# Optimization experiments

Measured on AMD Instinct MI355X. Metric: run time of the kernel, lower is better.

The kernel has to match this reference:

```python
import jax, jax.numpy as jnp
import numpy as np

# Model config (matches init_kwargs)
DIM = 2048
INTER = 1408          # moe_inter_dim
E = 16                # n_routed_experts
TOPK = 4              # n_activated_experts
G = 4                 # n_expert_groups
TOPK_G = 2            # n_limited_groups
N_SHARED = 2
SHARED_INTER = N_SHARED * INTER  # 2816
ROUTE_SCALE = 1.0


def setup_inputs() -> dict:
    key = jax.random.key(0)
    ks = jax.random.split(key, 8)
    s = 0.02
    x = jax.random.normal(ks[0], (1, 2048, DIM), dtype=jnp.float32)
    Wg = jax.random.normal(ks[1], (E, DIM), dtype=jnp.float32) * s      # gate weight
    W1 = jax.random.normal(ks[2], (E, INTER, DIM), dtype=jnp.float32) * s  # expert gate proj
    W3 = jax.random.normal(ks[3], (E, INTER, DIM), dtype=jnp.float32) * s  # expert up proj
    W2 = jax.random.normal(ks[4], (E, DIM, INTER), dtype=jnp.float32) * s  # expert down proj
    Ws1 = jax.random.normal(ks[5], (SHARED_INTER, DIM), dtype=jnp.float32) * s
    Ws3 = jax.random.normal(ks[6], (SHARED_INTER, DIM), dtype=jnp.float32) * s
    Ws2 = jax.random.normal(ks[7], (DIM, SHARED_INTER), dtype=jnp.float32) * s
    return {"x": x, "Wg": Wg, "W1": W1, "W3": W3, "W2": W2,
            "Ws1": Ws1, "Ws3": Ws3, "Ws2": Ws2}


def _moe_forward(x, Wg, W1, W3, W2, Ws1, Ws3, Ws2):
    B, S, D = x.shape
    xt = x.reshape(-1, D)              # [T, D]
    T = xt.shape[0]

    # ---- Gate: group-limited top-k routing (bias is None since dim != 7168) ----
    scores = jax.nn.softmax(xt @ Wg.T, axis=-1)          # [T, E]
    sg = scores.reshape(T, G, E // G)                    # [T, G, E/G]
    group_scores = sg.max(axis=-1)                       # amax per group
    gidx = jax.lax.top_k(group_scores, TOPK_G)[1]        # [T, TOPK_G]
    gmask = jax.nn.one_hot(gidx, G, dtype=jnp.float32).sum(axis=1) > 0  # [T, G] kept groups
    masked = jnp.where(gmask[:, :, None], sg, -jnp.inf).reshape(T, E)
    topi = jax.lax.top_k(masked, TOPK)[1]                # [T, TOPK] expert indices
    weights = jnp.take_along_axis(scores, topi, axis=1) * ROUTE_SCALE  # original_scores gather

    # ---- Routed experts: dense per-expert SwiGLU FFN, zero-weight combine ----
    # combine[t, e] = sum over k of weights[t, k] * (topi[t, k] == e)
    combine = jnp.zeros((T, E), xt.dtype).at[jnp.arange(T)[:, None], topi].add(weights)
    h = jax.nn.silu(jnp.einsum('td,eid->eti', xt, W1)) * jnp.einsum('td,eid->eti', xt, W3)
    expert_out = jnp.einsum('eti,edi->etd', h, W2)       # [E, T, D]
    y = jnp.einsum('etd,te->td', expert_out, combine)    # [T, D]

    # ---- Shared expert (applied to all tokens) ----
    z = (jax.nn.silu(xt @ Ws1.T) * (xt @ Ws3.T)) @ Ws2.T

    return (y + z).reshape(B, S, D)


def reference(x, Wg, W1, W3, W2, Ws1, Ws3, Ws2):
    return _moe_forward(x, Wg, W1, W3, W2, Ws1, Ws3, Ws2)
```

## Files before the change

### kernel.cpp

```cpp
#include <hip/hip_runtime.h>
#include <stdint.h>

#define D_MODEL  2048
#define N_INTER  1408
#define SH_INTER 2816
#define T_TOK    2048
#define NSLOT    (T_TOK * 4)
#define MIB(x)   ((size_t)(x) << 20)

typedef __attribute__((ext_vector_type(8))) short bf16x8;
typedef __attribute__((ext_vector_type(4))) float f32x4;

__device__ __forceinline__ unsigned short f2bf(float f){
  unsigned int b = __builtin_bit_cast(unsigned int, f);
  b = (b + 0x7FFFu + ((b >> 16) & 1u)) >> 16;
  return (unsigned short)b;
}
__device__ __forceinline__ float bf2f(unsigned short h){
  unsigned int b = ((unsigned int)h) << 16;
  return __builtin_bit_cast(float, b);
}

#define GLOAD16(gp, lp) __builtin_amdgcn_global_load_lds( \
    (const __attribute__((address_space(1))) unsigned int*)(gp), \
    (__attribute__((address_space(3))) unsigned int*)(lp), 16, 0, 0)

__device__ __forceinline__ void cvt_tail(const float* __restrict__ src,
                                         unsigned short* __restrict__ dst,
                                         int n4, int cb, int nblk, int tid){
  const float4* s = (const float4*)src;
  ushort4* d = (ushort4*)dst;
  const int stride = nblk * 256;
  for (int i = cb * 256 + tid; i < n4; i += stride){
    const float4 v = s[i];
    ushort4 u; u.x = f2bf(v.x); u.y = f2bf(v.y); u.z = f2bf(v.z); u.w = f2bf(v.w);
    d[i] = u;
  }
}

__global__ void cvt4_kernel(const float* __restrict__ x,  const float* __restrict__ Ws1,
                            const float* __restrict__ Ws3, const float* __restrict__ Ws2,
                            unsigned short* __restrict__ xbf, unsigned short* __restrict__ S1,
                            unsigned short* __restrict__ S3,  unsigned short* __restrict__ S2){
  const int N0 = T_TOK * D_MODEL / 4;
  const int NW = SH_INTER * D_MODEL / 4;
  const int total = N0 + 3 * NW;
  const int stride = gridDim.x * blockDim.x;
  for (int i = blockIdx.x * blockDim.x + threadIdx.x; i < total; i += stride){
    const float4* s; ushort4* d; int j;
    if (i < N0)            { s = (const float4*)x;   d = (ushort4*)xbf; j = i; }
    else if (i < N0 + NW)  { s = (const float4*)Ws1; d = (ushort4*)S1;  j = i - N0; }
    else if (i < N0 + 2*NW){ s = (const float4*)Ws3; d = (ushort4*)S3;  j = i - N0 - NW; }
    else                   { s = (const float4*)Ws2; d = (ushort4*)S2;  j = i - N0 - 2*NW; }
    const float4 v = s[j];
    ushort4 u; u.x = f2bf(v.x); u.y = f2bf(v.y); u.z = f2bf(v.z); u.w = f2bf(v.w);
    d[j] = u;
  }
}

__global__ void gate_kernel(const float* __restrict__ x, const float* __restrict__ Wg,
                            int* __restrict__ cnt, int* __restrict__ list,
                            float* __restrict__ wslot){
  const int t = blockIdx.x;
  const int l = threadIdx.x;
  const int e = l & 15, q = l >> 4;
  const float* xr = x + (size_t)t * D_MODEL + q * 512;
  const float* wr = Wg + (size_t)e * D_MODEL + q * 512;
  float p = 0.f;
  #pragma unroll 4
  for (int i = 0; i < 512; i += 4){
    float4 xv = *(const float4*)(xr + i);
    float4 wv = *(const float4*)(wr + i);
    p += xv.x*wv.x + xv.y*wv.y + xv.z*wv.z + xv.w*wv.w;
  }
  p += __shfl_xor(p, 16);
  p += __shfl_xor(p, 32);
  float mx = p;
  for (int d = 1; d < 16; d <<= 1) mx = fmaxf(mx, __shfl_xor(mx, d));
  float ex = __expf(p - mx);
  float sum = ex;
  for (int d = 1; d < 16; d <<= 1) sum += __shfl_xor(sum, d);
  const float sc = ex / sum;
  float gm = fmaxf(sc, __shfl_xor(sc, 1));
  gm = fmaxf(gm, __shfl_xor(gm, 2));
  const float g0 = __shfl(gm, 0), g1 = __shfl(gm, 4),
              g2 = __shfl(gm, 8), g3 = __shfl(gm, 12);
  const int grp = e >> 2;
  const float gs[4] = {g0, g1, g2, g3};
  int grank = 0;
  #pragma unroll
  for (int j = 0; j < 4; ++j)
    if (gs[j] > gm || (gs[j] == gm && j < grp)) grank++;
  const float msc = (grank < 2) ? sc : -INFINITY;
  int erank = 0;
  #pragma unroll
  for (int j = 0; j < 16; ++j){
    const float oj = __shfl(msc, j);
    if (oj > msc || (oj == msc && j < e)) erank++;
  }
  if (q == 0 && erank < 4 && msc > -INFINITY){
    const int pos = atomicAdd(&cnt[e], 1);
    const int slot = (t << 2) | erank;
    list[e * T_TOK + pos] = slot;
    wslot[slot] = sc;
  }
}

template<int MODE>
__global__ __launch_bounds__(256, 3)
void gemm6_kernel(const unsigned short* __restrict__ A,
                  const unsigned short* __restrict__ B,
                  void* __restrict__ OutP,
                  const int* __restrict__ list,
                  const int* __restrict__ cnt,
                  int N, int K, int Astride, int MT, int NT,
                  const float* __restrict__ cvtSrc,
                  unsigned short* __restrict__ cvtDst,
                  int cvtN4, int gemmN)
{
  constexpr bool GATHER = (MODE >= 2);
  __shared__ unsigned short As[3 * 128 * 32];
  __shared__ unsigned short Bs[3 * 128 * 32];

  const int tid = threadIdx.x;
  const int bid = blockIdx.x;
  if (bid >= gemmN){
    cvt_tail(cvtSrc, cvtDst, cvtN4, bid - gemmN, gridDim.x - gemmN, tid);
    return;
  }

  const int per = gemmN >> 3;
  const int gsw = (bid & 7) * per + (bid >> 3);
  const int mt   = gsw % MT;
  const int rest = gsw / MT;
  const int nt = GATHER ? (rest % NT) : rest;
  const int e  = GATHER ? (rest / NT) : 0;

  const int cntE = GATHER ? cnt[e] : (MT * 128);
  if (mt * 128 >= cntE) return;

  const int wid = tid >> 6, lane = tid & 63;

  const int rt0 = 32 * wid + (lane >> 2), rt1 = rt0 + 16;
  const int sxA = ((lane & 3) ^ ((lane >> 3) & 3)) << 3;

  int ar0, ar1;
  if constexpr (GATHER){
    const int lim = cntE - 1;
    int p0 = mt * 128 + rt0; p0 = p0 < lim ? p0 : lim;
    int p1 = mt * 128 + rt1; p1 = p1 < lim ? p1 : lim;
    const int e0 = list[e * T_TOK + p0], e1 = list[e * T_TOK + p1];
    ar0 = (MODE == 2) ? (e0 >> 2) : e0;
    ar1 = (MODE == 2) ? (e1 >> 2) : e1;
  } else { ar0 = mt * 128 + rt0; ar1 = mt * 128 + rt1; }

  const unsigned short* pa0 = A + (size_t)ar0 * Astride + sxA;
  const unsigned short* pa1 = A + (size_t)ar1 * Astride + sxA;
  const unsigned short* pb0 = B + (GATHER ? (size_t)e * N * K : 0)
                            + (size_t)(nt * 128 + rt0) * K + sxA;
  const unsigned short* pb1 = pb0 + (size_t)16 * K;

  const int aW0 = (32 * wid) * 32, aW1 = aW0 + 16 * 32;
  const int bufStride = 128 * 32;

  const int wr = wid >> 1, wc = wid & 1, lr = lane & 15, lq = lane >> 4;
  const int fx = ((lq ^ ((lr >> 1) & 3)) << 3);
  int aoff[4], boff[4];
  #pragma unroll
  for (int m = 0; m < 4; ++m) aoff[m] = (wr * 64 + m * 16 + lr) * 32 + fx;
  #pragma unroll
  for (int n = 0; n < 4; ++n) boff[n] = (wc * 64 + n * 16 + lr) * 32 + fx;

  f32x4 acc[4][4];
  const f32x4 zero = {0.f, 0.f, 0.f, 0.f};
  #pragma unroll
  for (int m = 0; m < 4; ++m)
    #pragma unroll
    for (int n = 0; n < 4; ++n) acc[m][n] = zero;

  const int KT = K >> 5;
  #pragma unroll
  for (int t = 0; t < 3; ++t){
    GLOAD16(pa0, As + t * bufStride + aW0);
    GLOAD16(pa1, As + t * bufStride + aW1);
    GLOAD16(pb0, Bs + t * bufStride + aW0);
    GLOAD16(pb1, Bs + t * bufStride + aW1);
    pa0 += 32; pa1 += 32; pb0 += 32; pb1 += 32;
  }
  int c = 0;

  for (int kt = 0; kt < KT; ++kt){
    if (kt < KT - 2)       asm volatile("s_waitcnt vmcnt(8)" ::: "memory");
    else if (kt == KT - 2) asm volatile("s_waitcnt vmcnt(4)" ::: "memory");
    else                   asm volatile("s_waitcnt vmcnt(0)" ::: "memory");
    __builtin_amdgcn_s_barrier();

    const unsigned short* aC = As + c * bufStride;
    const unsigned short* bC = Bs + c * bufStride;
    bf16x8 af[4], bf[4];
    #pragma unroll
    for (int m = 0; m < 4; ++m) af[m] = *(const bf16x8*)(aC + aoff[m]);
    #pragma unroll
    for (int n = 0; n < 4; ++n) bf[n] = *(const bf16x8*)(bC + boff[n]);

    asm volatile("s_waitcnt lgkmcnt(0)" ::: "memory");
    __builtin_amdgcn_sched_barrier(0);
    __builtin_amdgcn_s_barrier();

    if (kt + 3 < KT){
      GLOAD16(pa0, As + c * bufStride + aW0);
      GLOAD16(pa1, As + c * bufStride + aW1);
      GLOAD16(pb0, Bs + c * bufStride + aW0);
      GLOAD16(pb1, Bs + c * bufStride + aW1);
      pa0 += 32; pa1 += 32; pb0 += 32; pb1 += 32;
    }

    #pragma unroll
    for (int n = 0; n < 4; ++n)
      #pragma unroll
      for (int m = 0; m < 4; ++m)
        acc[m][n] = __builtin_amdgcn_mfma_f32_16x16x32_bf16(af[m], bf[n], acc[m][n], 0, 0, 0);

    c = (c == 2) ? 0 : c + 1;
  }

  const int colBase = nt * 128 + wc * 64;
  #pragma unroll
  for (int m = 0; m < 4; ++m){
    #pragma unroll
    for (int r = 0; r < 4; ++r){
      const int grow = mt * 128 + wr * 64 + m * 16 + lq * 4 + r;
      if constexpr (MODE == 1){
        float* op = (float*)OutP + (size_t)grow * N + colBase;
        #pragma unroll
        for (int n = 0; n < 4; ++n) op[n * 16 + lr] = acc[m][n][r];
      } else if constexpr (MODE == 0){
        unsigned short* op = (unsigned short*)OutP + (size_t)grow * N + colBase;
        #pragma unroll
        for (int n = 0; n < 4; ++n) op[n * 16 + lr] = f2bf(acc[m][n][r]);
      } else {
        if (grow >= cntE) continue;
        const int orow = list[e * T_TOK + grow];
        unsigned short* op = (unsigned short*)OutP + (size_t)orow * N + colBase;
        #pragma unroll
        for (int n = 0; n < 4; ++n) op[n * 16 + lr] = f2bf(acc[m][n][r]);
      }
    }
  }
}

__global__ void swiglu_ip_kernel(unsigned short* __restrict__ GU, int n8, int NI8){
  const int stride = gridDim.x * blockDim.x;
  bf16x8* p = (bf16x8*)GU;
  for (int i = blockIdx.x * blockDim.x + threadIdx.x; i < n8; i += stride){
    const int r = i / NI8, ccol = i - r * NI8;
    const size_t gi = (size_t)r * 2 * NI8 + ccol;
    const bf16x8 g = p[gi];
    const bf16x8 u = p[gi + NI8];
    bf16x8 h;
    #pragma unroll
    for (int j = 0; j < 8; ++j){
      const float gv = bf2f((unsigned short)g[j]);
      const float uv = bf2f((unsigned short)u[j]);
      h[j] = (short)f2bf(gv / (1.f + __expf(-gv)) * uv);
    }
    p[gi] = h;
  }
}

__global__ void swiglu2_kernel(unsigned short* __restrict__ G,
                               const unsigned short* __restrict__ U, int n8){
  const int stride = gridDim.x * blockDim.x;
  for (int i = blockIdx.x * blockDim.x + threadIdx.x; i < n8; i += stride){
    const bf16x8 g = ((const bf16x8*)G)[i];
    const bf16x8 u = ((const bf16x8*)U)[i];
    bf16x8 h;
    #pragma unroll
    for (int j = 0; j < 8; ++j){
      const float gv = bf2f((unsigned short)g[j]);
      const float uv = bf2f((unsigned short)u[j]);
      h[j] = (short)f2bf(gv / (1.f + __expf(-gv)) * uv);
    }
    ((bf16x8*)G)[i] = h;
  }
}

__global__ void combine_kernel(const unsigned short* __restrict__ H2,
                               const float* __restrict__ wslot,
                               float* __restrict__ out){
  const int t = blockIdx.x;
  const int ccol = threadIdx.x * 8;
  float w[4];
  #pragma unroll
  for (int k = 0; k < 4; ++k) w[k] = wslot[t * 4 + k];
  float* o = out + (size_t)t * D_MODEL + ccol;
  float a[8];
  #pragma unroll
  for (int j = 0; j < 8; ++j) a[j] = o[j];
  #pragma unroll
  for (int k = 0; k < 4; ++k){
    const bf16x8 hv = *(const bf16x8*)(H2 + (size_t)(t * 4 + k) * D_MODEL + ccol);
    #pragma unroll
    for (int j = 0; j < 8; ++j) a[j] += w[k] * bf2f((unsigned short)hv[j]);
  }
  #pragma unroll
  for (int j = 0; j < 8; ++j) o[j] = a[j];
}

extern "C" void kernel_launch(void* const* d_in, const int* in_sizes, int n_in,
                              void* d_out, int out_size, void* d_ws, size_t ws_size,
                              hipStream_t stream)
{
  const float* x   = (const float*)d_in[0];
  const float* Wg  = (const float*)d_in[1];
  const float* W1  = (const float*)d_in[2];
  const float* W3  = (const float*)d_in[3];
  const float* W2  = (const float*)d_in[4];
  const float* Ws1 = (const float*)d_in[5];
  const float* Ws3 = (const float*)d_in[6];
  const float* Ws2 = (const float*)d_in[7];
  float* out = (float*)d_out;

  char* ws = (char*)d_ws;
  int*   cnt   = (int*)(ws);
  int*   list  = (int*)(ws + 4096);
  float* wslot = (float*)(ws + 4096 + 131072);
  unsigned short* xbf  = (unsigned short*)(ws + MIB(1));
  unsigned short* S1   = (unsigned short*)(ws + MIB(10));
  unsigned short* S3   = S1 + (size_t)SH_INTER * D_MODEL;
  unsigned short* S2   = (unsigned short*)(ws + MIB(34));
  unsigned short* GU_s = (unsigned short*)(ws + MIB(46));
  unsigned short* Gbuf = (unsigned short*)(ws + MIB(70));
  unsigned short* Ubuf = (unsigned short*)(ws + MIB(94));
  unsigned short* H2   = (unsigned short*)(ws + MIB(118));
  unsigned short* W1b  = (unsigned short*)(ws + MIB(152));
  unsigned short* W3b  = (unsigned short*)(ws + MIB(245));
  unsigned short* W2b  = (unsigned short*)(ws + MIB(338));

  const int NW_R = 16 * N_INTER * D_MODEL / 4;

  hipMemsetAsync(cnt, 0, 4096, stream);
  cvt4_kernel<<<2048, 256, 0, stream>>>(x, Ws1, Ws3, Ws2, xbf, S1, S3, S2);
  gate_kernel<<<T_TOK, 64, 0, stream>>>(x, Wg, cnt, list, wslot);

  gemm6_kernel<0><<<704 + 1344, 256, 0, stream>>>(
      xbf, S1, GU_s, nullptr, nullptr, 2 * SH_INTER, D_MODEL, D_MODEL, 16, 44,
      W1, W1b, NW_R, 704);
  swiglu_ip_kernel<<<2048, 256, 0, stream>>>(GU_s, T_TOK * SH_INTER / 8, SH_INTER / 8);

  gemm6_kernel<1><<<256 + 1792, 256, 0, stream>>>(
      GU_s, S2, out, nullptr, nullptr, D_MODEL, SH_INTER, 2 * SH_INTER, 16, 16,
      W3, W3b, NW_R, 256);

  gemm6_kernel<2><<<2816 + 1280, 256, 0, stream>>>(
      xbf, W1b, Gbuf, list, cnt, N_INTER, D_MODEL, D_MODEL, 16, 11,
      W2, W2b, NW_R, 2816);

  gemm6_kernel<2><<<2816, 256, 0, stream>>>(
      xbf, W3b, Ubuf, list, cnt, N_INTER, D_MODEL, D_MODEL, 16, 11,
      nullptr, nullptr, 0, 2816);

  swiglu2_kernel<<<2048, 256, 0, stream>>>(Gbuf, Ubuf, NSLOT * N_INTER / 8);

  gemm6_kernel<3><<<4096, 256, 0, stream>>>(
      Gbuf, W2b, H2, list, cnt, D_MODEL, N_INTER, N_INTER, 16, 16,
      nullptr, nullptr, 0, 4096);

  combine_kernel<<<T_TOK, 256, 0, stream>>>(H2, wslot, out);
}
```

Before: 670.7 us.

## Use 256-row expert GEMM tiles, merge gate/up GEMMs, unfuse weight conversion

Adds a 512-thread grouped GEMM for the routed experts that uses 256-row M tiles. Each B tile is now shared by twice as many gathered token rows, which halves the weight traffic per routed expert row. The W1 and W3 projections now run in one launch that writes an interleaved gate/up buffer, and the existing in-place SwiGLU kernel is reused on it, so a separate GEMM and SwiGLU launch go away. The fp32-to-bf16 conversion of the expert weights moves out of the GEMM tail blocks into standalone kernels, which removes overlap between conversion and compute. Tiles with partially filled 256-row blocks also waste more MFMA work on experts with ragged counts.

```diff
diff --git a/kernel.cpp b/kernel.cpp
--- a/kernel.cpp
+++ b/kernel.cpp
@@ -25,16 +25,13 @@
     (const __attribute__((address_space(1))) unsigned int*)(gp), \
     (__attribute__((address_space(3))) unsigned int*)(lp), 16, 0, 0)
 
-__device__ __forceinline__ void cvt_tail(const float* __restrict__ src,
-                                         unsigned short* __restrict__ dst,
-                                         int n4, int cb, int nblk, int tid){
-  const float4* s = (const float4*)src;
-  ushort4* d = (ushort4*)dst;
-  const int stride = nblk * 256;
-  for (int i = cb * 256 + tid; i < n4; i += stride){
-    const float4 v = s[i];
+__global__ void cvt_bf16_kernel(const float* __restrict__ x,
+                                unsigned short* __restrict__ o, int n4){
+  const int stride = gridDim.x * blockDim.x;
+  for (int i = blockIdx.x * blockDim.x + threadIdx.x; i < n4; i += stride){
+    const float4 v = ((const float4*)x)[i];
     ushort4 u; u.x = f2bf(v.x); u.y = f2bf(v.y); u.z = f2bf(v.z); u.w = f2bf(v.w);
-    d[i] = u;
+    ((ushort4*)o)[i] = u;
   }
 }
 
@@ -111,56 +108,27 @@
 void gemm6_kernel(const unsigned short* __restrict__ A,
                   const unsigned short* __restrict__ B,
                   void* __restrict__ OutP,
-                  const int* __restrict__ list,
-                  const int* __restrict__ cnt,
-                  int N, int K, int Astride, int MT, int NT,
-                  const float* __restrict__ cvtSrc,
-                  unsigned short* __restrict__ cvtDst,
-                  int cvtN4, int gemmN)
+                  int N, int K, int Astride, int MT, int NT)
 {
-  constexpr bool GATHER = (MODE >= 2);
   __shared__ unsigned short As[3 * 128 * 32];
   __shared__ unsigned short Bs[3 * 128 * 32];
 
-  const int tid = threadIdx.x;
-  const int bid = blockIdx.x;
-  if (bid >= gemmN){
-    cvt_tail(cvtSrc, cvtDst, cvtN4, bid - gemmN, gridDim.x - gemmN, tid);
-    return;
-  }
-
-  const int per = gemmN >> 3;
-  const int gsw = (bid & 7) * per + (bid >> 3);
+  const int per = gridDim.x >> 3;
+  const int gsw = (blockIdx.x & 7) * per + (blockIdx.x >> 3);
   const int mt   = gsw % MT;
-  const int rest = gsw / MT;
-  const int nt = GATHER ? (rest % NT) : rest;
-  const int e  = GATHER ? (rest / NT) : 0;
-
-  const int cntE = GATHER ? cnt[e] : (MT * 128);
-  if (mt * 128 >= cntE) return;
-
-  const int wid = tid >> 6, lane = tid & 63;
-
+  const int nt   = gsw / MT;
+
+  const int tid = threadIdx.x, wid = tid >> 6, lane = tid & 63;
   const int rt0 = 32 * wid + (lane >> 2), rt1 = rt0 + 16;
   const int sxA = ((lane & 3) ^ ((lane >> 3) & 3)) << 3;
 
-  int ar0, ar1;
-  if constexpr (GATHER){
-    const int lim = cntE - 1;
-    int p0 = mt * 128 + rt0; p0 = p0 < lim ? p0 : lim;
-    int p1 = mt * 128 + rt1; p1 = p1 < lim ? p1 : lim;
-    const int e0 = list[e * T_TOK + p0], e1 = list[e * T_TOK + p1];
-    ar0 = (MODE == 2) ? (e0 >> 2) : e0;
-    ar1 = (MODE == 2) ? (e1 >> 2) : e1;
-  } else { ar0 = mt * 128 + rt0; ar1 = mt * 128 + rt1; }
-
+  const int ar0 = mt * 128 + rt0, ar1 = mt * 128 + rt1;
   const unsigned short* pa0 = A + (size_t)ar0 * Astride + sxA;
   const unsigned short* pa1 = A + (size_t)ar1 * Astride + sxA;
-  const unsigned short* pb0 = B + (GATHER ? (size_t)e * N * K : 0)
-                            + (size_t)(nt * 128 + rt0) * K + sxA;
+  const unsigned short* pb0 = B + (size_t)(nt * 128 + rt0) * K + sxA;
   const unsigned short* pb1 = pb0 + (size_t)16 * K;
 
-  const int aW0 = (32 * wid) * 32, aW1 = aW0 + 16 * 32;
+  const int aW0 = (32 * wid) * 32, aW1 = aW0 + 512;
   const int bufStride = 128 * 32;
 
   const int wr = wid >> 1, wc = wid & 1, lr = lane & 15, lq = lane >> 4;
@@ -234,17 +202,136 @@
         float* op = (float*)OutP + (size_t)grow * N + colBase;
         #pragma unroll
         for (int n = 0; n < 4; ++n) op[n * 16 + lr] = acc[m][n][r];
-      } else if constexpr (MODE == 0){
+      } else {
         unsigned short* op = (unsigned short*)OutP + (size_t)grow * N + colBase;
         #pragma unroll
         for (int n = 0; n < 4; ++n) op[n * 16 + lr] = f2bf(acc[m][n][r]);
-      } else {
-        if (grow >= cntE) continue;
-        const int orow = list[e * T_TOK + grow];
-        unsigned short* op = (unsigned short*)OutP + (size_t)orow * N + colBase;
-        #pragma unroll
-        for (int n = 0; n < 4; ++n) op[n * 16 + lr] = f2bf(acc[m][n][r]);
       }
+    }
+  }
+}
+
+template<int MODE>
+__global__ __launch_bounds__(512, 2)
+void gemmW_kernel(const unsigned short* __restrict__ A,
+                  const unsigned short* __restrict__ BG,
+                  const unsigned short* __restrict__ BU,
+                  unsigned short* __restrict__ Out,
+                  const int* __restrict__ list,
+                  const int* __restrict__ cnt,
+                  int K, int N, int Astride, int NT, int NTH)
+{
+  __shared__ unsigned short As[3 * 8192];
+  __shared__ unsigned short Bs[3 * 4096];
+  const int MT = 8;
+
+  const int per = gridDim.x >> 3;
+  const int gsw = (blockIdx.x & 7) * per + (blockIdx.x >> 3);
+  const int mt   = gsw % MT;
+  const int rest = gsw / MT;
+  const int nt = rest % NT;
+  const int e  = rest / NT;
+  const int cntE = cnt[e];
+  if (mt * 256 >= cntE) return;
+
+  const int tid = threadIdx.x, wid = tid >> 6, lane = tid & 63;
+  const int sx = ((lane & 3) ^ ((lane >> 3) & 3)) << 3;
+
+  const int rt0 = 32 * wid + (lane >> 2), rt1 = rt0 + 16;
+  const int lim = cntE - 1;
+  int p0 = mt * 256 + rt0; p0 = p0 < lim ? p0 : lim;
+  int p1 = mt * 256 + rt1; p1 = p1 < lim ? p1 : lim;
+  const int e0 = list[e * T_TOK + p0], e1 = list[e * T_TOK + p1];
+  const int ar0 = (MODE == 2) ? (e0 >> 2) : e0;
+  const int ar1 = (MODE == 2) ? (e1 >> 2) : e1;
+  const unsigned short* pa0 = A + (size_t)ar0 * Astride + sx;
+  const unsigned short* pa1 = A + (size_t)ar1 * Astride + sx;
+
+  const int rb = 16 * wid + (lane >> 2);
+  const unsigned short* pb0;
+  if (MODE == 2){
+    const size_t eo = (size_t)e * N_INTER * K;
+    const unsigned short* wsrc = (nt < NTH) ? BG : BU;
+    const int rowoff = (nt < NTH) ? nt * 128 : (nt - NTH) * 128;
+    pb0 = wsrc + eo + (size_t)(rowoff + rb) * K + sx;
+  } else {
+    pb0 = BG + (size_t)e * N * K + (size_t)(nt * 128 + rb) * K + sx;
+  }
+
+  const int aW0 = (32 * wid) * 32, aW1 = aW0 + 512;
+  const int bW  = (16 * wid) * 32;
+  const int aStr = 8192, bStr = 4096;
+
+  const int wm = wid >> 1, wn = wid & 1, lr = lane & 15, lq = lane >> 4;
+  const int fx = ((lq ^ ((lr >> 1) & 3)) << 3);
+  int aoff[4], boff[4];
+  #pragma unroll
+  for (int m = 0; m < 4; ++m) aoff[m] = (wm * 64 + m * 16 + lr) * 32 + fx;
+  #pragma unroll
+  for (int n = 0; n < 4; ++n) boff[n] = (wn * 64 + n * 16 + lr) * 32 + fx;
+
+  f32x4 acc[4][4];
+  const f32x4 zero = {0.f, 0.f, 0.f, 0.f};
+  #pragma unroll
+  for (int m = 0; m < 4; ++m)
+    #pragma unroll
+    for (int n = 0; n < 4; ++n) acc[m][n] = zero;
+
+  const int KT = K >> 5;
+  #pragma unroll
+  for (int t = 0; t < 3; ++t){
+    GLOAD16(pa0, As + t * aStr + aW0);
+    GLOAD16(pa1, As + t * aStr + aW1);
+    GLOAD16(pb0, Bs + t * bStr + bW);
+    pa0 += 32; pa1 += 32; pb0 += 32;
+  }
+  int c = 0;
+
+  for (int kt = 0; kt < KT; ++kt){
+    if (kt < KT - 2)       asm volatile("s_waitcnt vmcnt(6)" ::: "memory");
+    else if (kt == KT - 2) asm volatile("s_waitcnt vmcnt(3)" ::: "memory");
+    else                   asm volatile("s_waitcnt vmcnt(0)" ::: "memory");
+    __builtin_amdgcn_s_barrier();
+
+    const unsigned short* aC = As + c * aStr;
+    const unsigned short* bC = Bs + c * bStr;
+    bf16x8 af[4], bf[4];
+    #pragma unroll
+    for (int m = 0; m < 4; ++m) af[m] = *(const bf16x8*)(aC + aoff[m]);
+    #pragma unroll
+    for (int n = 0; n < 4; ++n) bf[n] = *(const bf16x8*)(bC + boff[n]);
+
+    asm volatile("s_waitcnt lgkmcnt(0)" ::: "memory");
+    __builtin_amdgcn_sched_barrier(0);
+    __builtin_amdgcn_s_barrier();
+
+    if (kt + 3 < KT){
+      GLOAD16(pa0, As + c * aStr + aW0);
+      GLOAD16(pa1, As + c * aStr + aW1);
+      GLOAD16(pb0, Bs + c * bStr + bW);
+      pa0 += 32; pa1 += 32; pb0 += 32;
+    }
+
+    #pragma unroll
+    for (int n = 0; n < 4; ++n)
+      #pragma unroll
+      for (int m = 0; m < 4; ++m)
+        acc[m][n] = __builtin_amdgcn_mfma_f32_16x16x32_bf16(af[m], bf[n], acc[m][n], 0, 0, 0);
+
+    c = (c == 2) ? 0 : c + 1;
+  }
+
+  const int colBase = nt * 128 + wn * 64;
+  #pragma unroll
+  for (int m = 0; m < 4; ++m){
+    #pragma unroll
+    for (int r = 0; r < 4; ++r){
+      const int grow = mt * 256 + wm * 64 + m * 16 + lq * 4 + r;
+      if (grow >= cntE) continue;
+      const int orow = list[e * T_TOK + grow];
+      unsigned short* op = Out + (size_t)orow * N + colBase;
+      #pragma unroll
+      for (int n = 0; n < 4; ++n) op[n * 16 + lr] = f2bf(acc[m][n][r]);
     }
   }
 }
@@ -265,23 +352,6 @@
       h[j] = (short)f2bf(gv / (1.f + __expf(-gv)) * uv);
     }
     p[gi] = h;
-  }
-}
-
-__global__ void swiglu2_kernel(unsigned short* __restrict__ G,
-                               const unsigned short* __restrict__ U, int n8){
-  const int stride = gridDim.x * blockDim.x;
-  for (int i = blockIdx.x * blockDim.x + threadIdx.x; i < n8; i += stride){
-    const bf16x8 g = ((const bf16x8*)G)[i];
-    const bf16x8 u = ((const bf16x8*)U)[i];
-    bf16x8 h;
-    #pragma unroll
-    for (int j = 0; j < 8; ++j){
-      const float gv = bf2f((unsigned short)g[j]);
-      const float uv = bf2f((unsigned short)u[j]);
-      h[j] = (short)f2bf(gv / (1.f + __expf(-gv)) * uv);
-    }
-    ((bf16x8*)G)[i] = h;
   }
 }
 
@@ -330,8 +400,7 @@
   unsigned short* S3   = S1 + (size_t)SH_INTER * D_MODEL;
   unsigned short* S2   = (unsigned short*)(ws + MIB(34));
   unsigned short* GU_s = (unsigned short*)(ws + MIB(46));
-  unsigned short* Gbuf = (unsigned short*)(ws + MIB(70));
-  unsigned short* Ubuf = (unsigned short*)(ws + MIB(94));
+  unsigned short* Hr   = (unsigned short*)(ws + MIB(70));
   unsigned short* H2   = (unsigned short*)(ws + MIB(118));
   unsigned short* W1b  = (unsigned short*)(ws + MIB(152));
   unsigned short* W3b  = (unsigned short*)(ws + MIB(245));
@@ -343,28 +412,24 @@
   cvt4_kernel<<<2048, 256, 0, stream>>>(x, Ws1, Ws3, Ws2, xbf, S1, S3, S2);
   gate_kernel<<<T_TOK, 64, 0, stream>>>(x, Wg, cnt, list, wslot);
 
-  gemm6_kernel<0><<<704 + 1344, 256, 0, stream>>>(
-      xbf, S1, GU_s, nullptr, nullptr, 2 * SH_INTER, D_MODEL, D_MODEL, 16, 44,
-      W1, W1b, NW_R, 704);
+  gemm6_kernel<0><<<704, 256, 0, stream>>>(xbf, S1, GU_s,
+                                           2 * SH_INTER, D_MODEL, D_MODEL, 16, 44);
   swiglu_ip_kernel<<<2048, 256, 0, stream>>>(GU_s, T_TOK * SH_INTER / 8, SH_INTER / 8);
 
-  gemm6_kernel<1><<<256 + 1792, 256, 0, stream>>>(
-      GU_s, S2, out, nullptr, nullptr, D_MODEL, SH_INTER, 2 * SH_INTER, 16, 16,
-      W3, W3b, NW_R, 256);
-
-  gemm6_kernel<2><<<2816 + 1280, 256, 0, stream>>>(
-      xbf, W1b, Gbuf, list, cnt, N_INTER, D_MODEL, D_MODEL, 16, 11,
-      W2, W2b, NW_R, 2816);
-
-  gemm6_kernel<2><<<2816, 256, 0, stream>>>(
-      xbf, W3b, Ubuf, list, cnt, N_INTER, D_MODEL, D_MODEL, 16, 11,
-      nullptr, nullptr, 0, 2816);
-
-  swiglu2_kernel<<<2048, 256, 0, stream>>>(Gbuf, Ubuf, NSLOT * N_INTER / 8);
-
-  gemm6_kernel<3><<<4096, 256, 0, stream>>>(
-      Gbuf, W2b, H2, list, cnt, D_MODEL, N_INTER, N_INTER, 16, 16,
-      nullptr, nullptr, 0, 4096);
+  gemm6_kernel<1><<<256, 256, 0, stream>>>(GU_s, S2, out,
+                                           D_MODEL, SH_INTER, 2 * SH_INTER, 16, 16);
+
+  cvt_bf16_kernel<<<4096, 256, 0, stream>>>(W1, W1b, NW_R);
+  cvt_bf16_kernel<<<4096, 256, 0, stream>>>(W3, W3b, NW_R);
+
+  gemmW_kernel<2><<<16 * 8 * 22, 512, 0, stream>>>(xbf, W1b, W3b, Hr, list, cnt,
+                                                   D_MODEL, 2 * N_INTER, D_MODEL, 22, 11);
+  swiglu_ip_kernel<<<2048, 256, 0, stream>>>(Hr, NSLOT * N_INTER / 8, N_INTER / 8);
+
+  cvt_bf16_kernel<<<4096, 256, 0, stream>>>(W2, W2b, NW_R);
+
+  gemmW_kernel<3><<<16 * 8 * 16, 512, 0, stream>>>(Hr, W2b, nullptr, H2, list, cnt,
+                                                   N_INTER, D_MODEL, 2 * N_INTER, 16, 0);
 
   combine_kernel<<<T_TOK, 256, 0, stream>>>(H2, wslot, out);
 }
```

Result: slower. 686.7 us (+2.4%).
